# Kernel tuning notes

Hardware: AMD Instinct MI355X
Metric: run time of the kernel (lower is better)

## Reference

```python
import jax, jax.numpy as jnp
import numpy as np

NHEAD = 8
HEAD_DIM = 32  # per-head dim d; C = NHEAD * HEAD_DIM = 256
NEG_INF = -1e9


def setup_inputs() -> dict:
    key = jax.random.key(0)
    k1, k2, k3, k4, k5 = jax.random.split(key, 5)
    B, L, C = 8, 1024, NHEAD * HEAD_DIM
    query = jax.random.normal(k1, (B, L, C), dtype=jnp.float32)
    key_t = jax.random.normal(k2, (B, L, C), dtype=jnp.float32)
    value = jax.random.normal(k3, (B, L, C), dtype=jnp.float32)
    hard_mask = jax.random.randint(k4, (B, L), 0, 2).astype(bool)
    bias = jax.random.normal(k5, (B, L, L), dtype=jnp.float32)
    return {"query": query, "key": key_t, "value": value,
            "hard_mask": hard_mask, "bias": bias}


def reference(query, key, value, hard_mask, bias):
    # Faithful to the hard-mask path: attention is computed only among
    # active tokens (hard_mask True); inactive positions pass `value` through.
    # Masking inactive KEYS with -inf in the softmax is mathematically
    # identical to the sort/gather/slice/SDPA/scatter-unsort in the original.
    B, L, C = query.shape
    H, D = NHEAD, HEAD_DIM
    scale = 1.0 / jnp.sqrt(jnp.asarray(D, query.dtype))

    def split_heads(t):  # (B, L, C) -> (B, H, L, D)
        return t.reshape(B, L, H, D).transpose(0, 2, 1, 3)

    q, k, v = split_heads(query), split_heads(key), split_heads(value)

    # scores: (B, H, Lq, Lk); bias broadcasts over heads
    scores = jnp.einsum('bhld,bhmd->bhlm', q, k) * scale + bias[:, None, :, :]
    scores = jnp.where(hard_mask[:, None, None, :], scores, NEG_INF)
    attn = jax.nn.softmax(scores, axis=-1)
    out = jnp.einsum('bhlm,bhmd->bhld', attn, v)          # (B, H, L, D)
    out = out.transpose(0, 2, 1, 3).reshape(B, L, C)      # (B, L, C)

    # inactive query positions return the raw value (scatter-back behavior)
    out = jnp.where(hard_mask[:, :, None], out, value)

    # torch.stack over per-item (1, L, C) results -> (B, 1, L, C)
    return out[:, None, :, :]
```

## Files before the change

kernel.cpp:

```cpp
#include <hip/hip_runtime.h>
#include <hip/hip_bf16.h>

#define B_    8
#define H_    8
#define L_    1024
#define D_    32
#define C_    256
#define NK    64

typedef __attribute__((ext_vector_type(8))) short bf16x8;
typedef __attribute__((ext_vector_type(4))) float f32x4;

__device__ inline unsigned short f2bf(float f) {
    union { float f; unsigned int u; } x; x.f = f;
    return (unsigned short)((x.u + 0x7fffu + ((x.u >> 16) & 1u)) >> 16);
}

__device__ inline unsigned int pk_bf16(float lo, float hi) {
    union { __hip_bfloat162 h; unsigned int u; } c;
    c.h = __float22bfloat162_rn(make_float2(lo, hi));
    return c.u;
}

__global__ __launch_bounds__(256) void prep_frag(
    const float* __restrict__ k, const float* __restrict__ v,
    unsigned short* __restrict__ kfrag, unsigned short* __restrict__ vfrag)
{
    const int tid = threadIdx.x;
    const int blk = blockIdx.x;
    const int bh = blk >> 4, c = blk & 15;
    const int b = bh >> 3, h = bh & 7;

    __shared__ float sKf[64 * 36];
    __shared__ float sVf[64 * 33];

    {
        const int row = tid >> 2, seg = tid & 3;
        const size_t src = (size_t)(b * L_ + c * 64 + row) * C_ + h * D_ + seg * 8;
        float4 a = *(const float4*)(k + src);
        float4 d = *(const float4*)(k + src + 4);
        *(float4*)(sKf + row * 36 + seg * 8) = a;
        *(float4*)(sKf + row * 36 + seg * 8 + 4) = d;
        float4 va = *(const float4*)(v + src);
        float4 vd = *(const float4*)(v + src + 4);
        float* vr = sVf + row * 33 + seg * 8;
        vr[0] = va.x; vr[1] = va.y; vr[2] = va.z; vr[3] = va.w;
        vr[4] = vd.x; vr[5] = vd.y; vr[6] = vd.z; vr[7] = vd.w;
    }
    __syncthreads();

    const int ln = tid & 63, u = tid >> 6;
    const int l16 = ln & 15, quad = ln >> 4;

    {
        const float* src = sKf + (u * 16 + l16) * 36 + quad * 8;
        float4 a = *(const float4*)src;
        float4 d = *(const float4*)(src + 4);
        uint4 o = { pk_bf16(a.x, a.y), pk_bf16(a.z, a.w),
                    pk_bf16(d.x, d.y), pk_bf16(d.z, d.w) };
        *(uint4*)(kfrag + (size_t)blk * 2048 + u * 512 + ln * 8) = o;
    }
    {
        const int s2 = u >> 1, nt = u & 1;
        float vals[8];
#pragma unroll
        for (int j = 0; j < 8; ++j)
            vals[j] = sVf[(s2 * 32 + quad * 8 + j) * 33 + nt * 16 + l16];
        uint4 o = { pk_bf16(vals[0], vals[1]), pk_bf16(vals[2], vals[3]),
                    pk_bf16(vals[4], vals[5]), pk_bf16(vals[6], vals[7]) };
        *(uint4*)(vfrag + (size_t)blk * 2048 + s2 * 1024 + nt * 512 + ln * 8) = o;
    }
}

__global__ __launch_bounds__(256, 4) void attn_fa(
    const float* __restrict__ q,
    const float* __restrict__ v,
    const int*   __restrict__ mask,
    const float* __restrict__ bias,
    const unsigned short* __restrict__ kfrag,
    const unsigned short* __restrict__ vfrag,
    float*       __restrict__ out)
{
    __shared__ float sMadd[L_];
    __shared__ float sS[4][16 * 68];

    const int tid  = threadIdx.x;
    const int wv   = tid >> 6;
    const int ln   = tid & 63;
    const int l16  = ln & 15;
    const int quad = ln >> 4;

    const int blk = blockIdx.x;
    const int h   = blk >> 7;
    const int rem = blk & 127;
    const int b   = rem >> 4;
    const int qt  = rem & 15;
    const int q0  = qt * 64 + wv * 16;
    const int bh  = b * H_ + h;

    const float scale = 0.17677669529663687f;

    {
        int4 m = ((const int4*)(mask + b * L_))[tid];
        sMadd[tid * 4 + 0] = m.x ? 0.f : -1e9f;
        sMadd[tid * 4 + 1] = m.y ? 0.f : -1e9f;
        sMadd[tid * 4 + 2] = m.z ? 0.f : -1e9f;
        sMadd[tid * 4 + 3] = m.w ? 0.f : -1e9f;
    }
    __syncthreads();

    bf16x8 qfrag;
    {
        const float* qp = q + ((size_t)(b * L_ + q0 + l16) * C_ + h * D_ + quad * 8);
        float4 a = ((const float4*)qp)[0];
        float4 c = ((const float4*)qp)[1];
        __align__(16) unsigned int u[4] = {
            pk_bf16(a.x * scale, a.y * scale), pk_bf16(a.z * scale, a.w * scale),
            pk_bf16(c.x * scale, c.y * scale), pk_bf16(c.z * scale, c.w * scale)};
        qfrag = *(const bf16x8*)u;
    }

    bf16x8 onesf;
#pragma unroll
    for (int i = 0; i < 8; ++i) onesf[i] = (short)0x3F80;

    const unsigned short* kf_base = kfrag + (size_t)bh * 32768 + ln * 8;
    const unsigned short* vf_base = vfrag + (size_t)bh * 32768 + ln * 8;
    const float* bias_row = bias + (size_t)(b * L_ + q0 + l16) * L_;
    float* const sSw   = &sS[wv][0];
    const float* sSrow = &sS[wv][0] + l16 * 68;

    f32x4 Oacc[2] = {{0.f,0.f,0.f,0.f},{0.f,0.f,0.f,0.f}};
    f32x4 Lacc    = {0.f,0.f,0.f,0.f};

    for (int c = 0; c < 16; ++c) {
        const int j0 = c * NK;

        const unsigned short* kp = kf_base + c * 2048;
        bf16x8 kf0 = *(const bf16x8*)(kp);
        bf16x8 kf1 = *(const bf16x8*)(kp + 512);
        bf16x8 kf2 = *(const bf16x8*)(kp + 1024);
        bf16x8 kf3 = *(const bf16x8*)(kp + 1536);

        f32x4 S[4];
        S[0] = __builtin_amdgcn_mfma_f32_16x16x32_bf16(qfrag, kf0, (f32x4){0.f,0.f,0.f,0.f}, 0, 0, 0);
        S[1] = __builtin_amdgcn_mfma_f32_16x16x32_bf16(qfrag, kf1, (f32x4){0.f,0.f,0.f,0.f}, 0, 0, 0);
        S[2] = __builtin_amdgcn_mfma_f32_16x16x32_bf16(qfrag, kf2, (f32x4){0.f,0.f,0.f,0.f}, 0, 0, 0);
        S[3] = __builtin_amdgcn_mfma_f32_16x16x32_bf16(qfrag, kf3, (f32x4){0.f,0.f,0.f,0.f}, 0, 0, 0);

#pragma unroll
        for (int nt = 0; nt < 4; ++nt)
#pragma unroll
            for (int r = 0; r < 4; ++r)
                sSw[(quad * 4 + r) * 68 + nt * 16 + l16] = S[nt][r];

        bf16x8 pf[2];
#pragma unroll
        for (int s2 = 0; s2 < 2; ++s2) {
            const float* sr = sSrow + s2 * 32 + quad * 8;
            float4 a0 = *(const float4*)(sr);
            float4 a1 = *(const float4*)(sr + 4);
            const float* bp = bias_row + j0 + s2 * 32 + quad * 8;
            float4 b0 = *(const float4*)(bp);
            float4 b1 = *(const float4*)(bp + 4);
            const float* mp = sMadd + j0 + s2 * 32 + quad * 8;
            float4 m0 = *(const float4*)(mp);
            float4 m1 = *(const float4*)(mp + 4);
            float p0 = __expf(a0.x + b0.x + m0.x);
            float p1 = __expf(a0.y + b0.y + m0.y);
            float p2 = __expf(a0.z + b0.z + m0.z);
            float p3 = __expf(a0.w + b0.w + m0.w);
            float p4 = __expf(a1.x + b1.x + m1.x);
            float p5 = __expf(a1.y + b1.y + m1.y);
            float p6 = __expf(a1.z + b1.z + m1.z);
            float p7 = __expf(a1.w + b1.w + m1.w);
            __align__(16) unsigned int u[4] = {
                pk_bf16(p0, p1), pk_bf16(p2, p3),
                pk_bf16(p4, p5), pk_bf16(p6, p7)};
            pf[s2] = *(const bf16x8*)u;
        }

        const unsigned short* vp = vf_base + c * 2048;
#pragma unroll
        for (int s2 = 0; s2 < 2; ++s2) {
            Lacc = __builtin_amdgcn_mfma_f32_16x16x32_bf16(pf[s2], onesf, Lacc, 0, 0, 0);
#pragma unroll
            for (int nt = 0; nt < 2; ++nt) {
                bf16x8 vfr = *(const bf16x8*)(vp + s2 * 1024 + nt * 512);
                Oacc[nt] = __builtin_amdgcn_mfma_f32_16x16x32_bf16(pf[s2], vfr, Oacc[nt], 0, 0, 0);
            }
        }
    }

#pragma unroll
    for (int r = 0; r < 4; ++r) {
        const int qrow = q0 + quad * 4 + r;
        const float inv = 1.f / Lacc[r];
        const bool active = (sMadd[qrow] == 0.f);
        const size_t base = (size_t)(b * L_ + qrow) * C_ + h * D_;
#pragma unroll
        for (int nt = 0; nt < 2; ++nt) {
            const size_t idx = base + nt * 16 + l16;
            out[idx] = active ? Oacc[nt][r] * inv : v[idx];
        }
    }
}

#define MQ    64
#define KSTR  48
#define VSTR  72

__global__ __launch_bounds__(256) void masked_attn_mfma(
    const float* __restrict__ q,
    const float* __restrict__ k,
    const float* __restrict__ v,
    const int*   __restrict__ mask,
    const float* __restrict__ bias,
    float*       __restrict__ out)
{
    __shared__ __align__(16) unsigned short sQ[MQ][KSTR];
    __shared__ __align__(16) unsigned short sKt[NK][KSTR];
    __shared__ __align__(16) unsigned short sVt[D_][VSTR];
    __shared__ __align__(16) unsigned short sP2[4][16][VSTR];
    __shared__ float sMadd2[NK];

    const int tid  = threadIdx.x;
    const int wv   = tid >> 6;
    const int ln   = tid & 63;
    const int l16  = ln & 15;
    const int quad = ln >> 4;

    const int blk = blockIdx.x;
    const int h   = blk & 7;
    const int qt  = (blk >> 3) & 15;
    const int b   = blk >> 7;
    const int q0  = qt * MQ;
    const float scale = 0.17677669529663687f;

    {
        const int row = tid >> 2, d0 = (tid & 3) * 8;
        const float* src = q + ((size_t)(b * L_ + q0 + row) * C_ + h * D_ + d0);
        float4 a = ((const float4*)src)[0];
        float4 c = ((const float4*)src)[1];
        __align__(16) unsigned short t8[8] = {
            f2bf(a.x), f2bf(a.y), f2bf(a.z), f2bf(a.w),
            f2bf(c.x), f2bf(c.y), f2bf(c.z), f2bf(c.w)};
        *(int4*)&sQ[row][d0] = *(const int4*)t8;
    }
    __syncthreads();

    const bf16x8 qfrag = *(const bf16x8*)&sQ[wv * 16 + l16][quad * 8];
    f32x4 Oacc[2] = {{0.f,0.f,0.f,0.f},{0.f,0.f,0.f,0.f}};
    float lsum[4] = {0.f, 0.f, 0.f, 0.f};

    for (int j0 = 0; j0 < L_; j0 += NK) {
        __syncthreads();
        {
            const int row = tid >> 2, d0 = (tid & 3) * 8;
            const size_t src = (size_t)(b * L_ + j0 + row) * C_ + h * D_ + d0;
            float4 ka = ((const float4*)(k + src))[0];
            float4 kb = ((const float4*)(k + src))[1];
            __align__(16) unsigned short t8[8] = {
                f2bf(ka.x), f2bf(ka.y), f2bf(ka.z), f2bf(ka.w),
                f2bf(kb.x), f2bf(kb.y), f2bf(kb.z), f2bf(kb.w)};
            *(int4*)&sKt[row][d0] = *(const int4*)t8;

            float4 va = ((const float4*)(v + src))[0];
            float4 vb = ((const float4*)(v + src))[1];
            sVt[d0 + 0][row] = f2bf(va.x);
            sVt[d0 + 1][row] = f2bf(va.y);
            sVt[d0 + 2][row] = f2bf(va.z);
            sVt[d0 + 3][row] = f2bf(va.w);
            sVt[d0 + 4][row] = f2bf(vb.x);
            sVt[d0 + 5][row] = f2bf(vb.y);
            sVt[d0 + 6][row] = f2bf(vb.z);
            sVt[d0 + 7][row] = f2bf(vb.w);
            if (tid < NK) sMadd2[tid] = mask[b * L_ + j0 + tid] ? 0.f : -1e9f;
        }
        __syncthreads();

        bf16x8 kf[4];
#pragma unroll
        for (int nt = 0; nt < 4; ++nt)
            kf[nt] = *(const bf16x8*)&sKt[nt * 16 + l16][quad * 8];

        f32x4 S[4];
#pragma unroll
        for (int nt = 0; nt < 4; ++nt)
            S[nt] = __builtin_amdgcn_mfma_f32_16x16x32_bf16(
                qfrag, kf[nt], (f32x4){0.f,0.f,0.f,0.f}, 0, 0, 0);

        float psum[4] = {0.f, 0.f, 0.f, 0.f};
        const size_t brow0 = (size_t)(b * L_ + q0 + wv * 16 + quad * 4) * L_ + j0;
#pragma unroll
        for (int nt = 0; nt < 4; ++nt) {
            const float madd = sMadd2[nt * 16 + l16];
#pragma unroll
            for (int r = 0; r < 4; ++r) {
                float s = S[nt][r] * scale + bias[brow0 + (size_t)r * L_ + nt * 16 + l16] + madd;
                float p = __expf(s);
                psum[r] += p;
                S[nt][r] = p;
            }
        }
#pragma unroll
        for (int nt = 0; nt < 4; ++nt)
#pragma unroll
            for (int r = 0; r < 4; ++r)
                sP2[wv][quad * 4 + r][nt * 16 + l16] = f2bf(S[nt][r]);
#pragma unroll
        for (int r = 0; r < 4; ++r) {
            float t = psum[r];
            t += __shfl_xor(t, 1);
            t += __shfl_xor(t, 2);
            t += __shfl_xor(t, 4);
            t += __shfl_xor(t, 8);
            lsum[r] += t;
        }
#pragma unroll
        for (int s2 = 0; s2 < 2; ++s2) {
            bf16x8 pf = *(const bf16x8*)&sP2[wv][l16][s2 * 32 + quad * 8];
#pragma unroll
            for (int nt = 0; nt < 2; ++nt) {
                bf16x8 vf = *(const bf16x8*)&sVt[nt * 16 + l16][s2 * 32 + quad * 8];
                Oacc[nt] = __builtin_amdgcn_mfma_f32_16x16x32_bf16(pf, vf, Oacc[nt], 0, 0, 0);
            }
        }
    }
#pragma unroll
    for (int r = 0; r < 4; ++r) {
        const int qg = q0 + wv * 16 + quad * 4 + r;
        const int active = mask[b * L_ + qg];
        const size_t obase = (size_t)(b * L_ + qg) * C_ + h * D_;
        const float inv = 1.f / lsum[r];
#pragma unroll
        for (int nt = 0; nt < 2; ++nt) {
            float val;
            if (active) val = Oacc[nt][r] * inv;
            else        val = v[obase + nt * 16 + l16];
            out[obase + nt * 16 + l16] = val;
        }
    }
}

extern "C" void kernel_launch(void* const* d_in, const int* in_sizes, int n_in,
                              void* d_out, int out_size, void* d_ws, size_t ws_size,
                              hipStream_t stream) {
    const float* q    = (const float*)d_in[0];
    const float* k    = (const float*)d_in[1];
    const float* v    = (const float*)d_in[2];
    const int*   mask = (const int*)d_in[3];
    const float* bias = (const float*)d_in[4];
    float* out = (float*)d_out;

    if (ws_size >= (size_t)8 * 1024 * 1024) {
        unsigned short* kfrag = (unsigned short*)d_ws;
        unsigned short* vfrag = kfrag + (size_t)2 * 1024 * 1024;
        prep_frag<<<1024, 256, 0, stream>>>(k, v, kfrag, vfrag);
        attn_fa<<<1024, 256, 0, stream>>>(q, v, mask, bias, kfrag, vfrag, out);
    } else {
        masked_attn_mfma<<<1024, 256, 0, stream>>>(q, k, v, mask, bias, out);
    }
}
```

Measured before the change: 144.3 us.

## Precompute bias+mask as bf16 MFMA fragments and prefetch K/bias across chunks

A merged prep kernel now also converts the fp32 bias plus additive mask into bf16 laid out in MFMA accumulator order. The 8 heads then read bias at half the bytes and with no per-head mask add. The attention kernel adds bias straight to the S registers, so the fp32 S round-trip through LDS is gone, and only bf16 P is staged in LDS. It also software-prefetches the next chunk's K and bias fragments. The cost is an extra 16 MB workspace write plus read, a larger workspace threshold, and bf16 rounding of the bias, which affects accuracy.

```diff
diff --git a/kernel.cpp b/kernel.cpp
--- a/kernel.cpp
+++ b/kernel.cpp
@@ -7,6 +7,7 @@
 #define D_    32
 #define C_    256
 #define NK    64
+#define PSTR  72
 
 typedef __attribute__((ext_vector_type(8))) short bf16x8;
 typedef __attribute__((ext_vector_type(4))) float f32x4;
@@ -22,67 +23,102 @@
     return c.u;
 }
 
-__global__ __launch_bounds__(256) void prep_frag(
+__global__ __launch_bounds__(256) void prep_all(
     const float* __restrict__ k, const float* __restrict__ v,
-    unsigned short* __restrict__ kfrag, unsigned short* __restrict__ vfrag)
+    const float* __restrict__ bias, const int* __restrict__ mask,
+    unsigned short* __restrict__ kfrag, unsigned short* __restrict__ vfrag,
+    unsigned short* __restrict__ bfrag)
 {
     const int tid = threadIdx.x;
     const int blk = blockIdx.x;
-    const int bh = blk >> 4, c = blk & 15;
-    const int b = bh >> 3, h = bh & 7;
-
     __shared__ float sKf[64 * 36];
     __shared__ float sVf[64 * 33];
-
-    {
-        const int row = tid >> 2, seg = tid & 3;
-        const size_t src = (size_t)(b * L_ + c * 64 + row) * C_ + h * D_ + seg * 8;
-        float4 a = *(const float4*)(k + src);
-        float4 d = *(const float4*)(k + src + 4);
-        *(float4*)(sKf + row * 36 + seg * 8) = a;
-        *(float4*)(sKf + row * 36 + seg * 8 + 4) = d;
-        float4 va = *(const float4*)(v + src);
-        float4 vd = *(const float4*)(v + src + 4);
-        float* vr = sVf + row * 33 + seg * 8;
-        vr[0] = va.x; vr[1] = va.y; vr[2] = va.z; vr[3] = va.w;
-        vr[4] = vd.x; vr[5] = vd.y; vr[6] = vd.z; vr[7] = vd.w;
-    }
-    __syncthreads();
-
-    const int ln = tid & 63, u = tid >> 6;
-    const int l16 = ln & 15, quad = ln >> 4;
-
-    {
-        const float* src = sKf + (u * 16 + l16) * 36 + quad * 8;
-        float4 a = *(const float4*)src;
-        float4 d = *(const float4*)(src + 4);
-        uint4 o = { pk_bf16(a.x, a.y), pk_bf16(a.z, a.w),
-                    pk_bf16(d.x, d.y), pk_bf16(d.z, d.w) };
-        *(uint4*)(kfrag + (size_t)blk * 2048 + u * 512 + ln * 8) = o;
-    }
-    {
-        const int s2 = u >> 1, nt = u & 1;
-        float vals[8];
-#pragma unroll
-        for (int j = 0; j < 8; ++j)
-            vals[j] = sVf[(s2 * 32 + quad * 8 + j) * 33 + nt * 16 + l16];
-        uint4 o = { pk_bf16(vals[0], vals[1]), pk_bf16(vals[2], vals[3]),
-                    pk_bf16(vals[4], vals[5]), pk_bf16(vals[6], vals[7]) };
-        *(uint4*)(vfrag + (size_t)blk * 2048 + s2 * 1024 + nt * 512 + ln * 8) = o;
-    }
-}
-
-__global__ __launch_bounds__(256, 4) void attn_fa(
+    __shared__ float sMadd[L_];
+
+    if (blk < 1024) {
+        const int bh = blk >> 4, c = blk & 15;
+        const int b = bh >> 3, h = bh & 7;
+        {
+            const int row = tid >> 2, seg = tid & 3;
+            const size_t src = (size_t)(b * L_ + c * 64 + row) * C_ + h * D_ + seg * 8;
+            float4 a = *(const float4*)(k + src);
+            float4 d = *(const float4*)(k + src + 4);
+            *(float4*)(sKf + row * 36 + seg * 8) = a;
+            *(float4*)(sKf + row * 36 + seg * 8 + 4) = d;
+            float4 va = *(const float4*)(v + src);
+            float4 vd = *(const float4*)(v + src + 4);
+            float* vr = sVf + row * 33 + seg * 8;
+            vr[0] = va.x; vr[1] = va.y; vr[2] = va.z; vr[3] = va.w;
+            vr[4] = vd.x; vr[5] = vd.y; vr[6] = vd.z; vr[7] = vd.w;
+        }
+        __syncthreads();
+        const int ln = tid & 63, u = tid >> 6;
+        const int l16 = ln & 15, quad = ln >> 4;
+        {
+            const float* src = sKf + (u * 16 + l16) * 36 + quad * 8;
+            float4 a = *(const float4*)src;
+            float4 d = *(const float4*)(src + 4);
+            uint4 o = { pk_bf16(a.x, a.y), pk_bf16(a.z, a.w),
+                        pk_bf16(d.x, d.y), pk_bf16(d.z, d.w) };
+            *(uint4*)(kfrag + (size_t)blk * 2048 + u * 512 + ln * 8) = o;
+        }
+        {
+            const int s2 = u >> 1, nt = u & 1;
+            float vals[8];
+#pragma unroll
+            for (int j = 0; j < 8; ++j)
+                vals[j] = sVf[(s2 * 32 + quad * 8 + j) * 33 + nt * 16 + l16];
+            uint4 o = { pk_bf16(vals[0], vals[1]), pk_bf16(vals[2], vals[3]),
+                        pk_bf16(vals[4], vals[5]), pk_bf16(vals[6], vals[7]) };
+            *(uint4*)(vfrag + (size_t)blk * 2048 + s2 * 1024 + nt * 512 + ln * 8) = o;
+        }
+    } else {
+        const int bblk = blk - 1024;
+        const int b = bblk >> 6, strip = bblk & 63;
+        const int wv = tid >> 6, ln = tid & 63;
+        const int l16 = ln & 15, quad = ln >> 4;
+        {
+            int4 m = ((const int4*)(mask + b * L_))[tid];
+            sMadd[tid * 4 + 0] = m.x ? 0.f : -1e9f;
+            sMadd[tid * 4 + 1] = m.y ? 0.f : -1e9f;
+            sMadd[tid * 4 + 2] = m.z ? 0.f : -1e9f;
+            sMadd[tid * 4 + 3] = m.w ? 0.f : -1e9f;
+        }
+        __syncthreads();
+        const float* brow = bias + ((size_t)(b * L_) + strip * 16 + quad * 4) * L_;
+        unsigned short* obase = bfrag + (size_t)bblk * 16384;
+#pragma unroll
+        for (int cc = 0; cc < 4; ++cc) {
+            const int c = wv * 4 + cc;
+            float vals[16];
+#pragma unroll
+            for (int nt = 0; nt < 4; ++nt) {
+                const int col = c * 64 + nt * 16 + l16;
+                const float madd = sMadd[col];
+#pragma unroll
+                for (int r = 0; r < 4; ++r)
+                    vals[nt * 4 + r] = brow[(size_t)r * L_ + col] + madd;
+            }
+            uint4 o0 = { pk_bf16(vals[0],  vals[1]),  pk_bf16(vals[2],  vals[3]),
+                         pk_bf16(vals[4],  vals[5]),  pk_bf16(vals[6],  vals[7]) };
+            uint4 o1 = { pk_bf16(vals[8],  vals[9]),  pk_bf16(vals[10], vals[11]),
+                         pk_bf16(vals[12], vals[13]), pk_bf16(vals[14], vals[15]) };
+            *(uint4*)(obase + c * 1024 +   0 + ln * 8) = o0;
+            *(uint4*)(obase + c * 1024 + 512 + ln * 8) = o1;
+        }
+    }
+}
+
+__global__ __launch_bounds__(256, 4) void attn_fa2(
     const float* __restrict__ q,
     const float* __restrict__ v,
     const int*   __restrict__ mask,
-    const float* __restrict__ bias,
     const unsigned short* __restrict__ kfrag,
     const unsigned short* __restrict__ vfrag,
+    const unsigned short* __restrict__ bfrag,
     float*       __restrict__ out)
 {
-    __shared__ float sMadd[L_];
-    __shared__ float sS[4][16 * 68];
+    __shared__ __align__(16) unsigned short sP[4][16 * PSTR];
 
     const int tid  = threadIdx.x;
     const int wv   = tid >> 6;
@@ -95,19 +131,11 @@
     const int rem = blk & 127;
     const int b   = rem >> 4;
     const int qt  = rem & 15;
-    const int q0  = qt * 64 + wv * 16;
+    const int strip = qt * 4 + wv;
+    const int q0  = strip * 16;
     const int bh  = b * H_ + h;
 
     const float scale = 0.17677669529663687f;
-
-    {
-        int4 m = ((const int4*)(mask + b * L_))[tid];
-        sMadd[tid * 4 + 0] = m.x ? 0.f : -1e9f;
-        sMadd[tid * 4 + 1] = m.y ? 0.f : -1e9f;
-        sMadd[tid * 4 + 2] = m.z ? 0.f : -1e9f;
-        sMadd[tid * 4 + 3] = m.w ? 0.f : -1e9f;
-    }
-    __syncthreads();
 
     bf16x8 qfrag;
     {
@@ -126,77 +154,82 @@
 
     const unsigned short* kf_base = kfrag + (size_t)bh * 32768 + ln * 8;
     const unsigned short* vf_base = vfrag + (size_t)bh * 32768 + ln * 8;
-    const float* bias_row = bias + (size_t)(b * L_ + q0 + l16) * L_;
-    float* const sSw   = &sS[wv][0];
-    const float* sSrow = &sS[wv][0] + l16 * 68;
+    const unsigned short* bm_base = bfrag + (size_t)(b * 64 + strip) * 16384 + ln * 8;
+    unsigned short* const sPw = &sP[wv][0];
 
     f32x4 Oacc[2] = {{0.f,0.f,0.f,0.f},{0.f,0.f,0.f,0.f}};
     f32x4 Lacc    = {0.f,0.f,0.f,0.f};
 
+    bf16x8 kf[4];
+    uint4  bm[2];
+#pragma unroll
+    for (int nt = 0; nt < 4; ++nt)
+        kf[nt] = *(const bf16x8*)(kf_base + nt * 512);
+    bm[0] = *(const uint4*)(bm_base);
+    bm[1] = *(const uint4*)(bm_base + 512);
+
     for (int c = 0; c < 16; ++c) {
-        const int j0 = c * NK;
-
-        const unsigned short* kp = kf_base + c * 2048;
-        bf16x8 kf0 = *(const bf16x8*)(kp);
-        bf16x8 kf1 = *(const bf16x8*)(kp + 512);
-        bf16x8 kf2 = *(const bf16x8*)(kp + 1024);
-        bf16x8 kf3 = *(const bf16x8*)(kp + 1536);
+        bf16x8 vf[4];
+#pragma unroll
+        for (int u2 = 0; u2 < 4; ++u2)
+            vf[u2] = *(const bf16x8*)(vf_base + c * 2048 + u2 * 512);
 
         f32x4 S[4];
-        S[0] = __builtin_amdgcn_mfma_f32_16x16x32_bf16(qfrag, kf0, (f32x4){0.f,0.f,0.f,0.f}, 0, 0, 0);
-        S[1] = __builtin_amdgcn_mfma_f32_16x16x32_bf16(qfrag, kf1, (f32x4){0.f,0.f,0.f,0.f}, 0, 0, 0);
-        S[2] = __builtin_amdgcn_mfma_f32_16x16x32_bf16(qfrag, kf2, (f32x4){0.f,0.f,0.f,0.f}, 0, 0, 0);
-        S[3] = __builtin_amdgcn_mfma_f32_16x16x32_bf16(qfrag, kf3, (f32x4){0.f,0.f,0.f,0.f}, 0, 0, 0);
-
-#pragma unroll
-        for (int nt = 0; nt < 4; ++nt)
-#pragma unroll
-            for (int r = 0; r < 4; ++r)
-                sSw[(quad * 4 + r) * 68 + nt * 16 + l16] = S[nt][r];
-
-        bf16x8 pf[2];
+#pragma unroll
+        for (int nt = 0; nt < 4; ++nt)
+            S[nt] = __builtin_amdgcn_mfma_f32_16x16x32_bf16(
+                qfrag, kf[nt], (f32x4){0.f,0.f,0.f,0.f}, 0, 0, 0);
+
+        const int cn = (c < 15) ? c + 1 : 15;
+        bf16x8 kfN[4];
+        uint4  bmN[2];
+#pragma unroll
+        for (int nt = 0; nt < 4; ++nt)
+            kfN[nt] = *(const bf16x8*)(kf_base + cn * 2048 + nt * 512);
+        bmN[0] = *(const uint4*)(bm_base + cn * 1024);
+        bmN[1] = *(const uint4*)(bm_base + cn * 1024 + 512);
+
+        unsigned short* dst0 = sPw + quad * 4 * PSTR + l16;
+#pragma unroll
+        for (int nt = 0; nt < 4; ++nt) {
+            const unsigned int w0 = ((const unsigned int*)&bm[nt >> 1])[(nt & 1) * 2 + 0];
+            const unsigned int w1 = ((const unsigned int*)&bm[nt >> 1])[(nt & 1) * 2 + 1];
+            const float b0 = __uint_as_float(w0 << 16);
+            const float b1 = __uint_as_float(w0 & 0xffff0000u);
+            const float b2 = __uint_as_float(w1 << 16);
+            const float b3 = __uint_as_float(w1 & 0xffff0000u);
+            const float p0 = __expf(S[nt][0] + b0);
+            const float p1 = __expf(S[nt][1] + b1);
+            const float p2 = __expf(S[nt][2] + b2);
+            const float p3 = __expf(S[nt][3] + b3);
+            const unsigned int plo = pk_bf16(p0, p1);
+            const unsigned int phi = pk_bf16(p2, p3);
+            unsigned short* d = dst0 + nt * 16;
+            d[0 * PSTR] = (unsigned short)plo;
+            d[1 * PSTR] = (unsigned short)(plo >> 16);
+            d[2 * PSTR] = (unsigned short)phi;
+            d[3 * PSTR] = (unsigned short)(phi >> 16);
+        }
+
 #pragma unroll
         for (int s2 = 0; s2 < 2; ++s2) {
-            const float* sr = sSrow + s2 * 32 + quad * 8;
-            float4 a0 = *(const float4*)(sr);
-            float4 a1 = *(const float4*)(sr + 4);
-            const float* bp = bias_row + j0 + s2 * 32 + quad * 8;
-            float4 b0 = *(const float4*)(bp);
-            float4 b1 = *(const float4*)(bp + 4);
-            const float* mp = sMadd + j0 + s2 * 32 + quad * 8;
-            float4 m0 = *(const float4*)(mp);
-            float4 m1 = *(const float4*)(mp + 4);
-            float p0 = __expf(a0.x + b0.x + m0.x);
-            float p1 = __expf(a0.y + b0.y + m0.y);
-            float p2 = __expf(a0.z + b0.z + m0.z);
-            float p3 = __expf(a0.w + b0.w + m0.w);
-            float p4 = __expf(a1.x + b1.x + m1.x);
-            float p5 = __expf(a1.y + b1.y + m1.y);
-            float p6 = __expf(a1.z + b1.z + m1.z);
-            float p7 = __expf(a1.w + b1.w + m1.w);
-            __align__(16) unsigned int u[4] = {
-                pk_bf16(p0, p1), pk_bf16(p2, p3),
-                pk_bf16(p4, p5), pk_bf16(p6, p7)};
-            pf[s2] = *(const bf16x8*)u;
-        }
-
-        const unsigned short* vp = vf_base + c * 2048;
-#pragma unroll
-        for (int s2 = 0; s2 < 2; ++s2) {
-            Lacc = __builtin_amdgcn_mfma_f32_16x16x32_bf16(pf[s2], onesf, Lacc, 0, 0, 0);
-#pragma unroll
-            for (int nt = 0; nt < 2; ++nt) {
-                bf16x8 vfr = *(const bf16x8*)(vp + s2 * 1024 + nt * 512);
-                Oacc[nt] = __builtin_amdgcn_mfma_f32_16x16x32_bf16(pf[s2], vfr, Oacc[nt], 0, 0, 0);
-            }
-        }
+            bf16x8 pf = *(const bf16x8*)(sPw + l16 * PSTR + s2 * 32 + quad * 8);
+            Lacc = __builtin_amdgcn_mfma_f32_16x16x32_bf16(pf, onesf, Lacc, 0, 0, 0);
+            Oacc[0] = __builtin_amdgcn_mfma_f32_16x16x32_bf16(pf, vf[s2 * 2 + 0], Oacc[0], 0, 0, 0);
+            Oacc[1] = __builtin_amdgcn_mfma_f32_16x16x32_bf16(pf, vf[s2 * 2 + 1], Oacc[1], 0, 0, 0);
+        }
+
+#pragma unroll
+        for (int nt = 0; nt < 4; ++nt) kf[nt] = kfN[nt];
+        bm[0] = bmN[0];
+        bm[1] = bmN[1];
     }
 
 #pragma unroll
     for (int r = 0; r < 4; ++r) {
         const int qrow = q0 + quad * 4 + r;
+        const int active = mask[b * L_ + qrow];
         const float inv = 1.f / Lacc[r];
-        const bool active = (sMadd[qrow] == 0.f);
         const size_t base = (size_t)(b * L_ + qrow) * C_ + h * D_;
 #pragma unroll
         for (int nt = 0; nt < 2; ++nt) {
@@ -353,11 +386,12 @@
     const float* bias = (const float*)d_in[4];
     float* out = (float*)d_out;
 
-    if (ws_size >= (size_t)8 * 1024 * 1024) {
+    if (ws_size >= (size_t)24 * 1024 * 1024) {
         unsigned short* kfrag = (unsigned short*)d_ws;
         unsigned short* vfrag = kfrag + (size_t)2 * 1024 * 1024;
-        prep_frag<<<1024, 256, 0, stream>>>(k, v, kfrag, vfrag);
-        attn_fa<<<1024, 256, 0, stream>>>(q, v, mask, bias, kfrag, vfrag, out);
+        unsigned short* bfrag = vfrag + (size_t)2 * 1024 * 1024;
+        prep_all<<<1536, 256, 0, stream>>>(k, v, bias, mask, kfrag, vfrag, bfrag);
+        attn_fa2<<<1024, 256, 0, stream>>>(q, v, mask, kfrag, vfrag, bfrag, out);
     } else {
         masked_attn_mfma<<<1024, 256, 0, stream>>>(q, k, v, mask, bias, out);
     }
```

Result: faster. 127.3 us (-11.8%).
